# Performance work log

Hardware: AMD Instinct MI355X
Metric: run time of the kernel (lower is better)

## Reference

```python
import jax, jax.numpy as jnp
import numpy as np
from jax import lax

T = 8            # num_segments
NUM_HEADS = 4
DILATIONS = (1, 2)
EPS = 1e-5


def _conv2d(x, w, b):
    y = lax.conv_general_dilated(x, w, window_strides=(1, 1), padding=((1, 1), (1, 1)),
                                 dimension_numbers=('NCHW', 'OIHW', 'NCHW'))
    return y + b[None, :, None, None]


def _conv3d_gate(x, w, b, d):
    # grouped conv3d: C in, 2 out, kernel (3,3,3), dilation (d,1,1), padding (d,1,1), groups=2
    y = lax.conv_general_dilated(x, w, window_strides=(1, 1, 1),
                                 padding=((d, d), (1, 1), (1, 1)),
                                 rhs_dilation=(d, 1, 1),
                                 dimension_numbers=('NCDHW', 'OIDHW', 'NCDHW'),
                                 feature_group_count=2)
    return y + b[None, :, None, None, None]


def _shift_time(y, s, left):
    # y: [B, C/2, T, H, W]; roll along time axis with zero padding
    B, C2, Tn, H, W = y.shape
    z = jnp.zeros((B, C2, s, H, W), y.dtype)
    if left:
        return jnp.concatenate([y[:, :, s:], z], axis=2)
    return jnp.concatenate([z, y[:, :, :Tn - s]], axis=2)


def _shuffle(y):
    # view(B,2,C/4,T,H,W).permute(0,2,1,3,4,5).view(B,C/2,T,H,W): channel interleave
    B, C2, Tn, H, W = y.shape
    return y.reshape(B, 2, C2 // 2, Tn, H, W).transpose(0, 2, 1, 3, 4, 5).reshape(B, C2, Tn, H, W)


def _fuse(x, w, b, d):
    # x: [B, C, T, H, W]
    Cc = x.shape[1]
    gate = jnp.tanh(_conv3d_gate(x, w, b, d))          # [B, 2, T, H, W]
    g1, g2 = gate[:, :1], gate[:, 1:2]
    x1, x2 = x[:, :Cc // 2], x[:, Cc // 2:]
    y1 = g1 * x1
    y2 = g2 * x2
    y1 = _shift_time(y1, d, True) + (x1 - y1)          # shifted gated part + residual
    y2 = _shift_time(y2, d, False) + (x2 - y2)
    y = jnp.concatenate([_shuffle(y1), _shuffle(y2)], axis=1)  # [B, C, T, H, W]
    B, Cc2, Tn, H, W = y.shape
    return y.transpose(0, 2, 1, 3, 4).reshape(B * Tn, Cc2, H, W)


def setup_inputs() -> dict:
    key = jax.random.key(0)
    ks = jax.random.split(key, 4)
    BT, C, H, W = 32, 256, 56, 56
    x = jax.random.normal(ks[0], (BT, C, H, W), jnp.float32)
    attn_w = jax.random.normal(ks[1], (NUM_HEADS, C, 3, 3), jnp.float32) * 0.05
    attn_b = jnp.zeros((NUM_HEADS,), jnp.float32)
    gate_w0 = jax.random.normal(ks[2], (2, C // 2, 3, 3, 3), jnp.float32) * 0.05
    gate_b0 = jnp.zeros((2,), jnp.float32)
    gate_w1 = jax.random.normal(ks[3], (2, C // 2, 3, 3, 3), jnp.float32) * 0.05
    gate_b1 = jnp.zeros((2,), jnp.float32)
    bn_gamma = jnp.ones((C,), jnp.float32)
    bn_beta = jnp.zeros((C,), jnp.float32)
    alpha = jnp.ones((2,), jnp.float32)
    return {"x": x, "attn_w": attn_w, "attn_b": attn_b, "bn_gamma": bn_gamma,
            "bn_beta": bn_beta, "gate_w0": gate_w0, "gate_b0": gate_b0,
            "gate_w1": gate_w1, "gate_b1": gate_b1, "alpha": alpha}


def reference(x, attn_w, attn_b, bn_gamma, bn_beta, gate_w0, gate_b0, gate_w1, gate_b1, alpha):
    BT, C, H, W = x.shape
    B = BT // T
    # multi-head spatial attention gating
    attn = jax.nn.sigmoid(jax.nn.relu(_conv2d(x, attn_w, attn_b)))  # [BT, nh, H, W]
    xh = x.reshape(BT, NUM_HEADS, C // NUM_HEADS, H, W) * attn[:, :, None]
    x5 = xh.reshape(B, T, C, H, W).transpose(0, 2, 1, 3, 4)         # [B, C, T, H, W]
    # BatchNorm3d (training-mode batch stats) + ReLU
    mean = x5.mean(axis=(0, 2, 3, 4), keepdims=True)
    var = x5.var(axis=(0, 2, 3, 4), keepdims=True)
    xn = (x5 - mean) * lax.rsqrt(var + EPS)
    xn = xn * bn_gamma[None, :, None, None, None] + bn_beta[None, :, None, None, None]
    xr = jax.nn.relu(xn)
    out = (alpha[0] * _fuse(xr, gate_w0, gate_b0, DILATIONS[0])
           + alpha[1] * _fuse(xr, gate_w1, gate_b1, DILATIONS[1]))
    return out
```

## Files before the change

### kernel.cpp

```cpp
#include <hip/hip_runtime.h>
#include <math.h>

#define HH 56
#define WW 56
#define CC 256
#define TT 8
#define HW 3136

__global__ __launch_bounds__(256)
void k1_attn(const float* __restrict__ x, const float* __restrict__ aw,
             float* __restrict__ attn_raw) {
    const int blk = blockIdx.x;
    const int cs  = blk & 3;
    const int ht  = (blk >> 2) % 14;
    const int bt  = blk / 56;
    const int h0  = ht * 4;
    __shared__ float tile[2][6 * 58];
    float* tf = &tile[0][0];
    const int tid = threadIdx.x;
    const float* xb = x + ((size_t)bt * CC + cs * 64) * HW;

    int  soff[2], goff[2];
    bool vld[2];
    #pragma unroll
    for (int k = 0; k < 2; ++k) {
        int idx = tid + k * 256;
        bool in = idx < 6 * 58;
        int r   = idx / 58;
        int col = idx - r * 58;
        int gh = h0 + r - 1, gw = col - 1;
        bool v = in && (unsigned)gh < HH && (unsigned)gw < WW;
        vld[k]  = v;
        soff[k] = idx;
        goff[k] = gh * WW + gw;
        if (in && !v) { tf[idx] = 0.f; tf[348 + idx] = 0.f; }
    }

    #pragma unroll
    for (int k = 0; k < 2; ++k)
        if (vld[k]) tf[soff[k]] = xb[goff[k]];
    __syncthreads();

    const int wc = tid % WW;
    const int hr = tid / WW;
    const bool active = tid < 4 * WW;
    float acc[4] = {0.f, 0.f, 0.f, 0.f};

    for (int cl = 0; cl < 64; ++cl) {
        float xv[2];
        if (cl < 63) {
            #pragma unroll
            for (int k = 0; k < 2; ++k)
                xv[k] = vld[k] ? xb[(size_t)(cl + 1) * HW + goff[k]] : 0.f;
        }
        if (active) {
            const float* buf = tf + (cl & 1) * 348;
            float v[9];
            #pragma unroll
            for (int ki = 0; ki < 3; ++ki)
                #pragma unroll
                for (int kj = 0; kj < 3; ++kj)
                    v[ki * 3 + kj] = buf[(hr + ki) * 58 + wc + kj];
            const int c = cs * 64 + cl;
            #pragma unroll
            for (int h = 0; h < 4; ++h) {
                const float* w = aw + ((size_t)h * CC + c) * 9;
                float s = 0.f;
                #pragma unroll
                for (int k = 0; k < 9; ++k) s = fmaf(w[k], v[k], s);
                acc[h] += s;
            }
        }
        if (cl < 63) {
            float* bufn = tf + ((cl + 1) & 1) * 348;
            #pragma unroll
            for (int k = 0; k < 2; ++k)
                if (vld[k]) bufn[soff[k]] = xv[k];
        }
        __syncthreads();
    }

    if (active) {
        const int base = (h0 + hr) * WW + wc;
        #pragma unroll
        for (int h = 0; h < 4; ++h)
            atomicAdd(&attn_raw[((size_t)bt * 4 + h) * HW + base], acc[h]);
    }
}

__global__ void k1b_act(const float* __restrict__ raw, const float* __restrict__ ab,
                        float* __restrict__ attn) {
    int i = blockIdx.x * 256 + threadIdx.x;
    if (i >= 32 * 4 * HW) return;
    int o = (i / HW) & 3;
    float z = fmaxf(raw[i] + ab[o], 0.f);
    attn[i] = 1.f / (1.f + expf(-z));
}

__global__ __launch_bounds__(256)
void k2_stats(const float* __restrict__ x, const float* __restrict__ attn,
              float* __restrict__ bn_sum, float* __restrict__ bn_sumsq) {
    const int c  = blockIdx.x & 255;
    const int bt = blockIdx.x >> 8;
    const int head = c >> 6;
    const float4* xp = (const float4*)(x + ((size_t)bt * CC + c) * HW);
    const float4* ap = (const float4*)(attn + ((size_t)bt * 4 + head) * HW);
    float s = 0.f, s2 = 0.f;
    for (int i = threadIdx.x; i < HW / 4; i += 256) {
        float4 xv = xp[i], av = ap[i];
        float v0 = xv.x * av.x, v1 = xv.y * av.y, v2 = xv.z * av.z, v3 = xv.w * av.w;
        s  += v0 + v1 + v2 + v3;
        s2 += v0 * v0 + v1 * v1 + v2 * v2 + v3 * v3;
    }
    #pragma unroll
    for (int off = 32; off > 0; off >>= 1) {
        s  += __shfl_down(s, off);
        s2 += __shfl_down(s2, off);
    }
    __shared__ float red[8];
    const int wave = threadIdx.x >> 6;
    if ((threadIdx.x & 63) == 0) { red[wave * 2] = s; red[wave * 2 + 1] = s2; }
    __syncthreads();
    if (threadIdx.x == 0) {
        atomicAdd(&bn_sum[c],   red[0] + red[2] + red[4] + red[6]);
        atomicAdd(&bn_sumsq[c], red[1] + red[3] + red[5] + red[7]);
    }
}

__global__ void k3_final(const float* __restrict__ bn_sum, const float* __restrict__ bn_sumsq,
                         const float* __restrict__ gamma, const float* __restrict__ beta,
                         float* __restrict__ scale, float* __restrict__ shift) {
    int c = threadIdx.x;
    const float invN = 1.f / 100352.f;
    float mean = bn_sum[c] * invN;
    float var  = bn_sumsq[c] * invN - mean * mean;
    float sc   = gamma[c] * rsqrtf(var + 1e-5f);
    scale[c] = sc;
    shift[c] = fmaf(-mean, sc, beta[c]);
}

__global__ __launch_bounds__(256)
void k4_gate(const float* __restrict__ x, const float* __restrict__ attn,
             const float* __restrict__ scale, const float* __restrict__ shift,
             const float* __restrict__ gw0, const float* __restrict__ gw1,
             float* __restrict__ gate_raw) {
    const int blk   = blockIdx.x;
    const int chunk = blk & 31;
    const int ht    = (blk >> 5) % 14;
    const int b     = blk / (32 * 14);
    const int h0    = ht * 4;
    const int g     = chunk >> 4;
    const int head  = chunk >> 3;
    __shared__ float tile[2][348 * 12];
    const int tid = threadIdx.x;

    int   pgoff[2];
    bool  pvld[2];
    float pav[2][8];
    #pragma unroll
    for (int k = 0; k < 2; ++k) {
        int p = tid + k * 256;
        bool in = p < 348;
        int r   = p / 58;
        int col = p - r * 58;
        int gh = h0 + r - 1, gw = col - 1;
        bool v = in && (unsigned)gh < HH && (unsigned)gw < WW;
        pvld[k]  = v;
        pgoff[k] = gh * WW + gw;
        #pragma unroll
        for (int t = 0; t < 8; ++t)
            pav[k][t] = v ? attn[((size_t)(b * 8 + t) * 4 + head) * HW + pgoff[k]] : 0.f;
        if (in && !v) {
            float4 z = make_float4(0.f, 0.f, 0.f, 0.f);
            *(float4*)&tile[0][p * 12]     = z;
            *(float4*)&tile[0][p * 12 + 4] = z;
            *(float4*)&tile[1][p * 12]     = z;
            *(float4*)&tile[1][p * 12 + 4] = z;
        }
    }

    {
        const int c0 = chunk * 8;
        const float sc = scale[c0], sh = shift[c0];
        #pragma unroll
        for (int k = 0; k < 2; ++k)
            if (pvld[k]) {
                float v[8];
                #pragma unroll
                for (int t = 0; t < 8; ++t) {
                    float xv = x[((size_t)((b * 8 + t) * CC + c0)) * HW + pgoff[k]];
                    v[t] = fmaxf(fmaf(xv * pav[k][t], sc, sh), 0.f);
                }
                int p = tid + k * 256;
                *(float4*)&tile[0][p * 12]     = make_float4(v[0], v[1], v[2], v[3]);
                *(float4*)&tile[0][p * 12 + 4] = make_float4(v[4], v[5], v[6], v[7]);
            }
    }
    __syncthreads();

    const int wc = tid % WW;
    const int hr = tid / WW;
    const bool active = tid < 4 * WW;
    float acc[2][8];
    #pragma unroll
    for (int d = 0; d < 2; ++d)
        #pragma unroll
        for (int t = 0; t < 8; ++t) acc[d][t] = 0.f;

    for (int cl = 0; cl < 8; ++cl) {
        const int c = chunk * 8 + cl;
        float xn[2][8];
        if (cl < 7) {
            #pragma unroll
            for (int k = 0; k < 2; ++k)
                if (pvld[k]) {
                    #pragma unroll
                    for (int t = 0; t < 8; ++t)
                        xn[k][t] = x[((size_t)((b * 8 + t) * CC + c + 1)) * HW + pgoff[k]];
                }
        }
        if (active) {
            const float* buf = &tile[cl & 1][0];
            const int ci = c & 127;
            const float* wp0 = gw0 + ((size_t)g * 128 + ci) * 27;
            const float* wp1 = gw1 + ((size_t)g * 128 + ci) * 27;
            #pragma unroll
            for (int ki = 0; ki < 3; ++ki) {
                #pragma unroll
                for (int kj = 0; kj < 3; ++kj) {
                    const int tap = ki * 3 + kj;
                    const int pos = (hr + ki) * 58 + wc + kj;
                    const float4 A = *(const float4*)(buf + pos * 12);
                    const float4 B = *(const float4*)(buf + pos * 12 + 4);
                    const float vv[8] = {A.x, A.y, A.z, A.w, B.x, B.y, B.z, B.w};
                    #pragma unroll
                    for (int kd = 0; kd < 3; ++kd) {
                        const float w0 = wp0[kd * 9 + tap];
                        const float w1 = wp1[kd * 9 + tap];
                        #pragma unroll
                        for (int t = 0; t < 8; ++t) {
                            const int to1 = t + 1 - kd;
                            if (to1 >= 0 && to1 < 8)
                                acc[0][to1] = fmaf(w0, vv[t], acc[0][to1]);
                            const int to2 = t + 2 - 2 * kd;
                            if (to2 >= 0 && to2 < 8)
                                acc[1][to2] = fmaf(w1, vv[t], acc[1][to2]);
                        }
                    }
                }
            }
        }
        if (cl < 7) {
            const float scn = scale[c + 1], shn = shift[c + 1];
            float* bufn = &tile[(cl + 1) & 1][0];
            #pragma unroll
            for (int k = 0; k < 2; ++k)
                if (pvld[k]) {
                    float v[8];
                    #pragma unroll
                    for (int t = 0; t < 8; ++t)
                        v[t] = fmaxf(fmaf(xn[k][t] * pav[k][t], scn, shn), 0.f);
                    int p = tid + k * 256;
                    *(float4*)&bufn[p * 12]     = make_float4(v[0], v[1], v[2], v[3]);
                    *(float4*)&bufn[p * 12 + 4] = make_float4(v[4], v[5], v[6], v[7]);
                }
        }
        __syncthreads();
    }

    if (active) {
        const int hw = (h0 + hr) * WW + wc;
        #pragma unroll
        for (int d = 0; d < 2; ++d)
            #pragma unroll
            for (int t = 0; t < 8; ++t)
                atomicAdd(&gate_raw[(((size_t)(d * 4 + b) * 2 + g) * 8 + t) * HW + hw],
                          acc[d][t]);
    }
}

__global__ void k4b_tanh(const float* __restrict__ raw, const float* __restrict__ gb0,
                         const float* __restrict__ gb1, float* __restrict__ gt) {
    int i = blockIdx.x * 256 + threadIdx.x;
    if (i >= 401408) return;
    int d   = i / 200704;
    int rem = i - d * 200704;
    int g   = (rem / 25088) & 1;
    float bias = (d == 0) ? gb0[g] : gb1[g];
    gt[i] = tanhf(raw[i] + bias);
}

__global__ __launch_bounds__(256)
void k5_fuse(const float* __restrict__ x, const float* __restrict__ attn,
             const float* __restrict__ scale, const float* __restrict__ shift,
             const float* __restrict__ gt, const float* __restrict__ alpha,
             float* __restrict__ out) {
    const int blk  = blockIdx.x;
    const int tile = blk % 13;
    const int c    = (blk / 13) & 255;
    const int b    = blk / (13 * 256);
    const int hw   = tile * 256 + threadIdx.x;
    if (hw >= HW) return;
    const int clo  = c & 127;
    const int cs   = (c & 128) | ((clo & 1) << 6) | (clo >> 1);
    const int g    = c >> 7;
    const int head = cs >> 6;
    const float sc = scale[cs], sh = shift[cs];
    float xr[8], G0[8], G1[8];
    #pragma unroll
    for (int t = 0; t < 8; ++t) {
        const int bti = b * 8 + t;
        float xv = x[((size_t)bti * CC + cs) * HW + hw];
        float av = attn[((size_t)bti * 4 + head) * HW + hw];
        xr[t] = fmaxf(fmaf(xv * av, sc, sh), 0.f);
        G0[t] = gt[(((size_t)(0 * 4 + b) * 2 + g) * 8 + t) * HW + hw];
        G1[t] = gt[(((size_t)(1 * 4 + b) * 2 + g) * 8 + t) * HW + hw];
    }
    const float a0 = alpha[0], a1 = alpha[1];
    #pragma unroll
    for (int t = 0; t < 8; ++t) {
        float v0, v1;
        if (g == 0) {
            v0 = xr[t] * (1.f - G0[t]) + (t + 1 < 8 ? G0[t + 1] * xr[t + 1] : 0.f);
            v1 = xr[t] * (1.f - G1[t]) + (t + 2 < 8 ? G1[t + 2] * xr[t + 2] : 0.f);
        } else {
            v0 = xr[t] * (1.f - G0[t]) + (t - 1 >= 0 ? G0[t - 1] * xr[t - 1] : 0.f);
            v1 = xr[t] * (1.f - G1[t]) + (t - 2 >= 0 ? G1[t - 2] * xr[t - 2] : 0.f);
        }
        out[((size_t)(b * 8 + t) * CC + c) * HW + hw] = fmaf(a0, v0, a1 * v1);
    }
}

extern "C" void kernel_launch(void* const* d_in, const int* in_sizes, int n_in,
                              void* d_out, int out_size, void* d_ws, size_t ws_size,
                              hipStream_t stream) {
    const float* x     = (const float*)d_in[0];
    const float* aw    = (const float*)d_in[1];
    const float* ab    = (const float*)d_in[2];
    const float* gamma = (const float*)d_in[3];
    const float* beta  = (const float*)d_in[4];
    const float* gw0   = (const float*)d_in[5];
    const float* gb0   = (const float*)d_in[6];
    const float* gw1   = (const float*)d_in[7];
    const float* gb1   = (const float*)d_in[8];
    const float* alpha = (const float*)d_in[9];
    float* out = (float*)d_out;
    float* ws  = (float*)d_ws;

    float* gate_raw = ws;
    float* attn_raw = ws + 401408;
    float* gate_t   = attn_raw;
    float* bn_sum   = ws + 802816;
    float* bn_sumsq = ws + 803072;
    float* attn     = ws + 803328;
    float* scale    = ws + 1204736;
    float* shift    = ws + 1204992;

    hipMemsetAsync(ws, 0, (size_t)(401408 + 401408 + 512) * sizeof(float), stream);

    k1_attn <<<dim3(1792),  dim3(256), 0, stream>>>(x, aw, attn_raw);
    k1b_act <<<dim3(1568),  dim3(256), 0, stream>>>(attn_raw, ab, attn);
    k2_stats<<<dim3(8192),  dim3(256), 0, stream>>>(x, attn, bn_sum, bn_sumsq);
    k3_final<<<dim3(1),     dim3(256), 0, stream>>>(bn_sum, bn_sumsq, gamma, beta, scale, shift);
    k4_gate <<<dim3(1792),  dim3(256), 0, stream>>>(x, attn, scale, shift, gw0, gw1, gate_raw);
    k4b_tanh<<<dim3(1568),  dim3(256), 0, stream>>>(gate_raw, gb0, gb1, gate_t);
    k5_fuse <<<dim3(13312), dim3(256), 0, stream>>>(x, attn, scale, shift, gate_t, alpha, out);
}
```

Baseline: 185.1 us.

## Replace shared-memory stencil tile with register rows and wave shuffles in attention conv

```diff
diff --git a/kernel.cpp b/kernel.cpp
--- a/kernel.cpp
+++ b/kernel.cpp
@@ -10,81 +10,83 @@
 __global__ __launch_bounds__(256)
 void k1_attn(const float* __restrict__ x, const float* __restrict__ aw,
              float* __restrict__ attn_raw) {
-    const int blk = blockIdx.x;
-    const int cs  = blk & 3;
-    const int ht  = (blk >> 2) % 14;
-    const int bt  = blk / 56;
-    const int h0  = ht * 4;
-    __shared__ float tile[2][6 * 58];
-    float* tf = &tile[0][0];
-    const int tid = threadIdx.x;
+    const int blk  = blockIdx.x;
+    const int cs   = blk & 3;
+    const int ht   = (blk >> 2) % 14;
+    const int bt   = blk / 56;
+    const int wave = threadIdx.x >> 6;
+    const int lane = threadIdx.x & 63;
+    const int row  = ht * 4 + wave;
+    const int col  = lane;
+    const bool live = col < WW;
+    const bool okm = row > 0, okp = row < HH - 1;
+    const int base = row * WW + col;
+    const int offm = okm ? base - WW : base;
+    const int offp = okp ? base + WW : base;
     const float* xb = x + ((size_t)bt * CC + cs * 64) * HW;
 
-    int  soff[2], goff[2];
-    bool vld[2];
-    #pragma unroll
-    for (int k = 0; k < 2; ++k) {
-        int idx = tid + k * 256;
-        bool in = idx < 6 * 58;
-        int r   = idx / 58;
-        int col = idx - r * 58;
-        int gh = h0 + r - 1, gw = col - 1;
-        bool v = in && (unsigned)gh < HH && (unsigned)gw < WW;
-        vld[k]  = v;
-        soff[k] = idx;
-        goff[k] = gh * WW + gw;
-        if (in && !v) { tf[idx] = 0.f; tf[348 + idx] = 0.f; }
-    }
-
-    #pragma unroll
-    for (int k = 0; k < 2; ++k)
-        if (vld[k]) tf[soff[k]] = xb[goff[k]];
-    __syncthreads();
-
-    const int wc = tid % WW;
-    const int hr = tid / WW;
-    const bool active = tid < 4 * WW;
-    float acc[4] = {0.f, 0.f, 0.f, 0.f};
-
-    for (int cl = 0; cl < 64; ++cl) {
-        float xv[2];
-        if (cl < 63) {
-            #pragma unroll
-            for (int k = 0; k < 2; ++k)
-                xv[k] = vld[k] ? xb[(size_t)(cl + 1) * HW + goff[k]] : 0.f;
-        }
-        if (active) {
-            const float* buf = tf + (cl & 1) * 348;
-            float v[9];
-            #pragma unroll
-            for (int ki = 0; ki < 3; ++ki)
-                #pragma unroll
-                for (int kj = 0; kj < 3; ++kj)
-                    v[ki * 3 + kj] = buf[(hr + ki) * 58 + wc + kj];
-            const int c = cs * 64 + cl;
-            #pragma unroll
-            for (int h = 0; h < 4; ++h) {
-                const float* w = aw + ((size_t)h * CC + c) * 9;
-                float s = 0.f;
-                #pragma unroll
-                for (int k = 0; k < 9; ++k) s = fmaf(w[k], v[k], s);
-                acc[h] += s;
+    float acc0 = 0.f, acc1 = 0.f, acc2 = 0.f, acc3 = 0.f;
+
+    float cm[4], cc[4], cp[4];
+    #pragma unroll
+    for (int j = 0; j < 4; ++j) {
+        const float* xp = xb + (size_t)j * HW;
+        cm[j] = (live && okm) ? xp[offm] : 0.f;
+        cc[j] = live ? xp[base] : 0.f;
+        cp[j] = (live && okp) ? xp[offp] : 0.f;
+    }
+
+    for (int it = 0; it < 16; ++it) {
+        float nm[4], nc[4], np[4];
+        if (it < 15) {
+            #pragma unroll
+            for (int j = 0; j < 4; ++j) {
+                const float* xp = xb + (size_t)(it * 4 + 4 + j) * HW;
+                nm[j] = (live && okm) ? xp[offm] : 0.f;
+                nc[j] = live ? xp[base] : 0.f;
+                np[j] = (live && okp) ? xp[offp] : 0.f;
             }
         }
-        if (cl < 63) {
-            float* bufn = tf + ((cl + 1) & 1) * 348;
-            #pragma unroll
-            for (int k = 0; k < 2; ++k)
-                if (vld[k]) bufn[soff[k]] = xv[k];
-        }
-        __syncthreads();
-    }
-
-    if (active) {
-        const int base = (h0 + hr) * WW + wc;
-        #pragma unroll
-        for (int h = 0; h < 4; ++h)
-            atomicAdd(&attn_raw[((size_t)bt * 4 + h) * HW + base], acc[h]);
+        const int c0 = cs * 64 + it * 4;
+        #pragma unroll
+        for (int j = 0; j < 4; ++j) {
+            float vm = cm[j], vc = cc[j], vp = cp[j];
+            float vml = __shfl_up(vm, 1), vcl = __shfl_up(vc, 1), vpl = __shfl_up(vp, 1);
+            if (lane == 0) { vml = 0.f; vcl = 0.f; vpl = 0.f; }
+            float vmr = __shfl_down(vm, 1), vcr = __shfl_down(vc, 1), vpr = __shfl_down(vp, 1);
+
+            const int c = c0 + j;
+            const float* w0 = aw + ((size_t)0 * CC + c) * 9;
+            const float* w1 = aw + ((size_t)1 * CC + c) * 9;
+            const float* w2 = aw + ((size_t)2 * CC + c) * 9;
+            const float* w3 = aw + ((size_t)3 * CC + c) * 9;
+
+            acc0 = fmaf(w0[0], vml, acc0); acc0 = fmaf(w0[1], vm, acc0); acc0 = fmaf(w0[2], vmr, acc0);
+            acc0 = fmaf(w0[3], vcl, acc0); acc0 = fmaf(w0[4], vc, acc0); acc0 = fmaf(w0[5], vcr, acc0);
+            acc0 = fmaf(w0[6], vpl, acc0); acc0 = fmaf(w0[7], vp, acc0); acc0 = fmaf(w0[8], vpr, acc0);
+
+            acc1 = fmaf(w1[0], vml, acc1); acc1 = fmaf(w1[1], vm, acc1); acc1 = fmaf(w1[2], vmr, acc1);
+            acc1 = fmaf(w1[3], vcl, acc1); acc1 = fmaf(w1[4], vc, acc1); acc1 = fmaf(w1[5], vcr, acc1);
+            acc1 = fmaf(w1[6], vpl, acc1); acc1 = fmaf(w1[7], vp, acc1); acc1 = fmaf(w1[8], vpr, acc1);
+
+            acc2 = fmaf(w2[0], vml, acc2); acc2 = fmaf(w2[1], vm, acc2); acc2 = fmaf(w2[2], vmr, acc2);
+            acc2 = fmaf(w2[3], vcl, acc2); acc2 = fmaf(w2[4], vc, acc2); acc2 = fmaf(w2[5], vcr, acc2);
+            acc2 = fmaf(w2[6], vpl, acc2); acc2 = fmaf(w2[7], vp, acc2); acc2 = fmaf(w2[8], vpr, acc2);
+
+            acc3 = fmaf(w3[0], vml, acc3); acc3 = fmaf(w3[1], vm, acc3); acc3 = fmaf(w3[2], vmr, acc3);
+            acc3 = fmaf(w3[3], vcl, acc3); acc3 = fmaf(w3[4], vc, acc3); acc3 = fmaf(w3[5], vcr, acc3);
+            acc3 = fmaf(w3[6], vpl, acc3); acc3 = fmaf(w3[7], vp, acc3); acc3 = fmaf(w3[8], vpr, acc3);
+        }
+        if (it < 15) {
+            #pragma unroll
+            for (int j = 0; j < 4; ++j) { cm[j] = nm[j]; cc[j] = nc[j]; cp[j] = np[j]; }
+        }
+    }
+    if (live) {
+        atomicAdd(&attn_raw[((size_t)bt * 4 + 0) * HW + base], acc0);
+        atomicAdd(&attn_raw[((size_t)bt * 4 + 1) * HW + base], acc1);
+        atomicAdd(&attn_raw[((size_t)bt * 4 + 2) * HW + base], acc2);
+        atomicAdd(&attn_raw[((size_t)bt * 4 + 3) * HW + base], acc3);
     }
 }
 
```

Result: faster. 174.7 us (-5.6%).
